# Optimization experiments

Hardware: AMD Instinct MI355X
Metric: run time of the kernel (lower is better)

Reference implementation:

```python
import jax, jax.numpy as jnp
import numpy as np

B, D, C = 512, 512, 100000
M1, M2, M3 = 1.0, 0.5, 0.0  # canonical ArcFace margins
EPS = 1e-12  # tf.nn.l2_normalize epsilon


def _l2norm(v, axis):
    return v * jax.lax.rsqrt(jnp.maximum(jnp.sum(v * v, axis=axis, keepdims=True), EPS))


def setup_inputs() -> dict:
    key = jax.random.key(0)
    k1, k2, k3 = jax.random.split(key, 3)
    x = jax.random.normal(k1, (B, D), dtype=jnp.float32)
    W = jax.random.normal(k2, (D, C), dtype=jnp.float32)
    label_idx = jax.random.randint(k3, (B,), 0, C, dtype=jnp.int32)
    return {"x": x, "W": W, "label_idx": label_idx}


def reference(x, W, label_idx):
    xn = _l2norm(x, axis=1)            # [B, D] unit embeddings
    Wn = _l2norm(W, axis=0)            # [D, C] unit class weights (norm=True fc)
    logits = xn @ Wn                   # [B, C] cosine similarities
    # gather target cosine per row (gather_nd over one-hot label)
    t = jnp.take_along_axis(logits, label_idx[:, None], axis=1)[:, 0]  # [B]
    # m1 == 1.0 -> skip angular scaling branch; m2 != 0 -> additive angular margin
    t = jnp.arccos(t) + M2
    # clamp to pi value-wise, straight-through gradient: t1 = t + pi - stop_grad(t)
    t = jnp.minimum(t, t + (jnp.pi - jax.lax.stop_gradient(t)))
    t = jnp.cos(t)
    onehot = jax.nn.one_hot(label_idx, C, dtype=logits.dtype)  # [B, C]
    out = logits * (1.0 - onehot) + t[:, None] * onehot
    out = out - onehot * M3
    return out
```

## Files before the change

### kernel.cpp

```cpp
#include <hip/hip_runtime.h>
#include <math.h>

#define BB 512
#define DD 512
#define CC 100000
#define MARGIN2 0.5f
#define PI_F 3.14159265358979323846f

#define BM 128
#define BN 128
#define BK 64
#define KSTEPS (DD / BK)
#define NPAN 782
#define GRID (4 * NPAN)

typedef __bf16 bf16x8 __attribute__((ext_vector_type(8)));
typedef float f32x4 __attribute__((ext_vector_type(4)));

static __device__ __forceinline__ unsigned short f2bf(float f) {
    union { float f; unsigned u; } v; v.f = f;
    unsigned r = v.u + 0x7FFFu + ((v.u >> 16) & 1u);
    return (unsigned short)(r >> 16);
}

static __device__ __forceinline__ int swz(int row, int kbyte) {
    return row * 128 + (kbyte ^ ((row & 7) << 4));
}

static __device__ __forceinline__ void gll16(const unsigned char* g, unsigned char* l) {
    __builtin_amdgcn_global_load_lds(
        (const __attribute__((address_space(1))) void*)g,
        (__attribute__((address_space(3))) void*)l, 16, 0, 0);
}

__global__ __launch_bounds__(256) void k_norm_x(const float* __restrict__ x,
                                                unsigned char* __restrict__ img) {
    const int lane = threadIdx.x & 63;
    const int row  = blockIdx.x * 4 + (threadIdx.x >> 6);
    const float* xr = x + (size_t)row * DD;
    float4 v0 = *(const float4*)(xr + lane * 4);
    float4 v1 = *(const float4*)(xr + lane * 4 + 256);
    float s = v0.x*v0.x + v0.y*v0.y + v0.z*v0.z + v0.w*v0.w
            + v1.x*v1.x + v1.y*v1.y + v1.z*v1.z + v1.w*v1.w;
    #pragma unroll
    for (int m = 32; m; m >>= 1) s += __shfl_xor(s, m, 64);
    float rs = rsqrtf(fmaxf(s, 1e-12f));
    ushort4 o0, o1;
    o0.x = f2bf(v0.x * rs); o0.y = f2bf(v0.y * rs);
    o0.z = f2bf(v0.z * rs); o0.w = f2bf(v0.w * rs);
    o1.x = f2bf(v1.x * rs); o1.y = f2bf(v1.y * rs);
    o1.z = f2bf(v1.z * rs); o1.w = f2bf(v1.w * rs);

    const int mb   = row >> 7;
    const int lrow = row & 127;
    const int k0   = lane * 4;
    const int t0   = k0 >> 6;
    const int c8   = (k0 >> 3) & 7;
    const int sub  = (k0 >> 2) & 1;
    const int base = (mb * 8 + t0) * 16384 + lrow * 128
                   + ((c8 * 16) ^ ((lrow & 7) << 4)) + sub * 8;
    *(ushort4*)(img + base)         = o0;
    *(ushort4*)(img + base + 65536) = o1;
}

#define ABUF 16384
#define LDSZ (2 * ABUF + 2 * 16384 + 512 + 512)

__global__ __launch_bounds__(512, 4) void k_gemm(const unsigned char* __restrict__ img,
                                                 const float* __restrict__ W,
                                                 const int* __restrict__ lab,
                                                 float* __restrict__ out) {
    __shared__ __align__(16) unsigned char LDS[LDSZ];
    unsigned char* bufA = LDS;
    unsigned char* bufB = LDS + 2 * ABUF;
    float* rn  = (float*)(LDS + 2 * ABUF + 32768);
    int*   labs = (int*)(LDS + 2 * ABUF + 32768 + 512);

    const int tid = threadIdx.x;
    const int bid = blockIdx.x;

    const int v  = (bid & 7) * 391 + (bid >> 3);
    const int mb = v & 3;
    const int nb = v >> 2;
    const int M0 = mb * BM;
    const int N0 = nb * BN;

    const int lane = tid & 63;
    const int wid  = tid >> 6;
    const int wm = wid >> 2;
    const int wn = wid & 3;
    const int lr = lane & 15;
    const int lg = lane >> 4;

    if (tid < 128) labs[tid] = lab[M0 + tid];

    int b_go[2], b_ld[2];
    #pragma unroll
    for (int i = 0; i < 2; ++i) {
        int s  = tid + i * 512;
        int n  = s & 127;
        int o  = s >> 7;
        int col = N0 + n;
        col = col < CC ? col : CC - 1;
        b_go[i] = o * 8 * CC + col;
        b_ld[i] = n * 128 + ((o * 16) ^ ((n & 7) << 4));
    }

    const unsigned char* imgA = img + mb * (8 * ABUF);
    const int lds_u = wid * 2048;

    float f0[2][8], f1[2][8], f2[2][8];
    float bsq[2] = {0.f, 0.f};

#define WAITV_(N) asm volatile("s_waitcnt vmcnt(" #N ")" ::: "memory")
#define WAITV(N) WAITV_(N)
#define SB() __builtin_amdgcn_sched_barrier(0)

#define LOAD_B(FR, T) do {                                                     \
    _Pragma("unroll")                                                          \
    for (int i = 0; i < 2; ++i) {                                              \
        const float* p = W + b_go[i] + (size_t)(T) * (BK * CC);                \
        _Pragma("unroll")                                                      \
        for (int j = 0; j < 8; ++j)                                            \
            FR[i][j] = p[(size_t)j * CC];                                      \
    } } while (0)

#define PACK_WRITE(FR, T) do {                                                 \
    unsigned char* dst = bufB + ((T) & 1) * 16384;                             \
    _Pragma("unroll")                                                          \
    for (int i = 0; i < 2; ++i) {                                              \
        _Pragma("unroll")                                                      \
        for (int j = 0; j < 8; ++j)                                            \
            bsq[i] += FR[i][j] * FR[i][j];                                     \
        uint4 w;                                                               \
        asm("v_cvt_pk_bf16_f32 %0, %1, %2" : "=v"(w.x) : "v"(FR[i][0]), "v"(FR[i][1])); \
        asm("v_cvt_pk_bf16_f32 %0, %1, %2" : "=v"(w.y) : "v"(FR[i][2]), "v"(FR[i][3])); \
        asm("v_cvt_pk_bf16_f32 %0, %1, %2" : "=v"(w.z) : "v"(FR[i][4]), "v"(FR[i][5])); \
        asm("v_cvt_pk_bf16_f32 %0, %1, %2" : "=v"(w.w) : "v"(FR[i][6]), "v"(FR[i][7])); \
        *(uint4*)(dst + b_ld[i]) = w;                                          \
    } } while (0)

#define GLL_A(T) do {                                                          \
    unsigned char* A_nxt = bufA + ((T) & 1) * ABUF;                            \
    const unsigned char* gsrc = imgA + (T) * ABUF;                             \
    gll16(gsrc + lds_u + lane * 16, A_nxt + lds_u);                            \
    gll16(gsrc + lds_u + 1024 + lane * 16, A_nxt + lds_u + 1024);              \
    } while (0)

#define COMPUTE(T) do {                                                        \
    const unsigned char* A_cur = bufA + ((T) & 1) * ABUF;                      \
    const unsigned char* B_cur = bufB + ((T) & 1) * 16384;                     \
    __builtin_amdgcn_s_setprio(1);                                             \
    _Pragma("unroll")                                                          \
    for (int ks = 0; ks < 2; ++ks) {                                           \
        bf16x8 af[4], bfr[2];                                                  \
        _Pragma("unroll")                                                      \
        for (int mf = 0; mf < 4; ++mf)                                         \
            af[mf] = *(const bf16x8*)(A_cur + swz(wm * 64 + mf * 16 + lr, ks * 64 + lg * 16)); \
        _Pragma("unroll")                                                      \
        for (int nf = 0; nf < 2; ++nf)                                         \
            bfr[nf] = *(const bf16x8*)(B_cur + swz(wn * 32 + nf * 16 + lr, ks * 64 + lg * 16)); \
        _Pragma("unroll")                                                      \
        for (int mf = 0; mf < 4; ++mf)                                         \
            _Pragma("unroll")                                                  \
            for (int nf = 0; nf < 2; ++nf)                                     \
                acc[mf][nf] = __builtin_amdgcn_mfma_f32_16x16x32_bf16(         \
                    bfr[nf], af[mf], acc[mf][nf], 0, 0, 0);                    \
    }                                                                          \
    __builtin_amdgcn_s_setprio(0);                                             \
    } while (0)

#define KBODY(T, FP, FN) do {                                                  \
    if ((T) + 1 < KSTEPS) GLL_A((T) + 1);         \
    if ((T) + 3 < KSTEPS) LOAD_B(FN, (T) + 3);                                 \
    COMPUTE(T);                                                                \
    if ((T) + 1 < KSTEPS) PACK_WRITE(FP, (T) + 1);                             \
    SB();                                                                      \
    if ((T) + 1 < KSTEPS) {                                                    \
        if ((T) + 3 < KSTEPS) { WAITV(16); } else { WAITV(0); }                \
        SB();                                                                  \
        asm volatile("s_waitcnt lgkmcnt(0)" ::: "memory"); SB();               \
        __builtin_amdgcn_s_barrier(); SB();                                    \
    } } while (0)

    f32x4 acc[4][2];
    #pragma unroll
    for (int mf = 0; mf < 4; ++mf)
        #pragma unroll
        for (int nf = 0; nf < 2; ++nf)
            acc[mf][nf] = (f32x4)0.f;

    LOAD_B(f0, 0);
    GLL_A(0);
    LOAD_B(f1, 1);
    PACK_WRITE(f0, 0);
    LOAD_B(f2, 2);
    SB();
    WAITV(32); SB();
    asm volatile("s_waitcnt lgkmcnt(0)" ::: "memory"); SB();
    __builtin_amdgcn_s_barrier(); SB();

    KBODY(0, f1, f0);
    KBODY(1, f2, f1);
    KBODY(2, f0, f2);
    KBODY(3, f1, f0);
    KBODY(4, f2, f1);
    KBODY(5, f0, f2);
    KBODY(6, f1, f0);
    KBODY(7, f2, f1);

    __syncthreads();
    float* part = (float*)bufB;
    #pragma unroll
    for (int i = 0; i < 2; ++i)
        part[tid + i * 512] = bsq[i];
    __syncthreads();
    if (tid < BN) {
        float s = 0.f;
        #pragma unroll
        for (int o = 0; o < 8; ++o)
            s += part[o * BN + tid];
        rn[tid] = rsqrtf(fmaxf(s, 1e-12f));
    }
    __syncthreads();

    float* stag = (float*)bufA;
    #pragma unroll
    for (int rd = 0; rd < 4; ++rd) {
        if (wm == (rd >> 1)) {
            #pragma unroll
            for (int f = 0; f < 2; ++f) {
                const int mf = (rd & 1) * 2 + f;
                const int ml = f * 16 + lr;
                #pragma unroll
                for (int nf = 0; nf < 2; ++nf) {
                    const int nl = wn * 32 + nf * 16 + lg * 4;
                    const f32x4 rn4 = *(const f32x4*)(rn + nl);
                    f32x4 o;
                    #pragma unroll
                    for (int r = 0; r < 4; ++r)
                        o[r] = acc[mf][nf][r] * rn4[r];
                    *(f32x4*)(stag + ml * 132 + nl) = o;
                }
            }
        }
        __syncthreads();
        if (tid < 32) {
            const int c   = labs[rd * 32 + tid];
            const int off = c - N0;
            if (off >= 0 && off < BN) {
                float val = stag[tid * 132 + off];
                val = fminf(fmaxf(val, -1.f), 1.f);
                float th = fminf(acosf(val) + MARGIN2, PI_F);
                stag[tid * 132 + off] = cosf(th);
            }
        }
        __syncthreads();
        #pragma unroll
        for (int j = tid; j < 1024; j += 512) {
            const int m = j >> 5;
            const int n = (j & 31) * 4;
            if (N0 + n + 4 <= CC) {
                f32x4 o = *(const f32x4*)(stag + m * 132 + n);
                __builtin_nontemporal_store(o,
                    (f32x4*)(out + (size_t)(M0 + rd * 32 + m) * CC + N0 + n));
            }
        }
        __syncthreads();
    }
}

extern "C" void kernel_launch(void* const* d_in, const int* in_sizes, int n_in,
                              void* d_out, int out_size, void* d_ws, size_t ws_size,
                              hipStream_t stream) {
    const float* x   = (const float*)d_in[0];
    const float* W   = (const float*)d_in[1];
    const int*   lab = (const int*)d_in[2];
    float* out = (float*)d_out;

    unsigned char* img = (unsigned char*)d_ws;

    k_norm_x<<<dim3(BB / 4), dim3(256), 0, stream>>>(x, img);
    k_gemm<<<dim3(GRID), dim3(512), 0, stream>>>(img, W, lab, out);
}
```

Before: 103.8 us.

## Load A fragments directly from global into registers, drop LDS A buffer

The normalized x matrix is now stored row-major in bf16, and each wave loads its MFMA A fragments straight from global memory into registers instead of staging them through swizzled LDS with global_load_lds. This frees LDS (the A double buffer is removed) and removes the LDS reads for A. The B prefetch depth drops from three register sets to two, and the explicit vmcnt waits are removed. The risk is exposed global latency on the A loads, now issued in the same k-step they are used, plus reduced W prefetch depth.

```diff
diff --git a/kernel.cpp b/kernel.cpp
--- a/kernel.cpp
+++ b/kernel.cpp
@@ -27,14 +27,8 @@
     return row * 128 + (kbyte ^ ((row & 7) << 4));
 }
 
-static __device__ __forceinline__ void gll16(const unsigned char* g, unsigned char* l) {
-    __builtin_amdgcn_global_load_lds(
-        (const __attribute__((address_space(1))) void*)g,
-        (__attribute__((address_space(3))) void*)l, 16, 0, 0);
-}
-
 __global__ __launch_bounds__(256) void k_norm_x(const float* __restrict__ x,
-                                                unsigned char* __restrict__ img) {
+                                                unsigned short* __restrict__ xnb) {
     const int lane = threadIdx.x & 63;
     const int row  = blockIdx.x * 4 + (threadIdx.x >> 6);
     const float* xr = x + (size_t)row * DD;
@@ -50,31 +44,20 @@
     o0.z = f2bf(v0.z * rs); o0.w = f2bf(v0.w * rs);
     o1.x = f2bf(v1.x * rs); o1.y = f2bf(v1.y * rs);
     o1.z = f2bf(v1.z * rs); o1.w = f2bf(v1.w * rs);
-
-    const int mb   = row >> 7;
-    const int lrow = row & 127;
-    const int k0   = lane * 4;
-    const int t0   = k0 >> 6;
-    const int c8   = (k0 >> 3) & 7;
-    const int sub  = (k0 >> 2) & 1;
-    const int base = (mb * 8 + t0) * 16384 + lrow * 128
-                   + ((c8 * 16) ^ ((lrow & 7) << 4)) + sub * 8;
-    *(ushort4*)(img + base)         = o0;
-    *(ushort4*)(img + base + 65536) = o1;
-}
-
-#define ABUF 16384
-#define LDSZ (2 * ABUF + 2 * 16384 + 512 + 512)
-
-__global__ __launch_bounds__(512, 4) void k_gemm(const unsigned char* __restrict__ img,
+    *(ushort4*)(xnb + (size_t)row * DD + lane * 4)       = o0;
+    *(ushort4*)(xnb + (size_t)row * DD + lane * 4 + 256) = o1;
+}
+
+#define LDSZ (2 * 16384 + 512 + 512)
+
+__global__ __launch_bounds__(512, 4) void k_gemm(const unsigned short* __restrict__ xnb,
                                                  const float* __restrict__ W,
                                                  const int* __restrict__ lab,
                                                  float* __restrict__ out) {
     __shared__ __align__(16) unsigned char LDS[LDSZ];
-    unsigned char* bufA = LDS;
-    unsigned char* bufB = LDS + 2 * ABUF;
-    float* rn  = (float*)(LDS + 2 * ABUF + 32768);
-    int*   labs = (int*)(LDS + 2 * ABUF + 32768 + 512);
+    unsigned char* bufB = LDS;
+    float* rn   = (float*)(LDS + 32768);
+    int*   labs = (int*)(LDS + 32768 + 512);
 
     const int tid = threadIdx.x;
     const int bid = blockIdx.x;
@@ -93,6 +76,11 @@
     const int lg = lane >> 4;
 
     if (tid < 128) labs[tid] = lab[M0 + tid];
+
+    const unsigned short* aptr0 = xnb + (size_t)(M0 + wm * 64 +  0 + lr) * DD + lg * 8;
+    const unsigned short* aptr1 = xnb + (size_t)(M0 + wm * 64 + 16 + lr) * DD + lg * 8;
+    const unsigned short* aptr2 = xnb + (size_t)(M0 + wm * 64 + 32 + lr) * DD + lg * 8;
+    const unsigned short* aptr3 = xnb + (size_t)(M0 + wm * 64 + 48 + lr) * DD + lg * 8;
 
     int b_go[2], b_ld[2];
     #pragma unroll
@@ -106,14 +94,10 @@
         b_ld[i] = n * 128 + ((o * 16) ^ ((n & 7) << 4));
     }
 
-    const unsigned char* imgA = img + mb * (8 * ABUF);
-    const int lds_u = wid * 2048;
-
-    float f0[2][8], f1[2][8], f2[2][8];
+    float f0[2][8], f1[2][8];
     float bsq[2] = {0.f, 0.f};
-
-#define WAITV_(N) asm volatile("s_waitcnt vmcnt(" #N ")" ::: "memory")
-#define WAITV(N) WAITV_(N)
+    bf16x8 af[4][2];
+
 #define SB() __builtin_amdgcn_sched_barrier(0)
 
 #define LOAD_B(FR, T) do {                                                     \
@@ -140,23 +124,23 @@
         *(uint4*)(dst + b_ld[i]) = w;                                          \
     } } while (0)
 
-#define GLL_A(T) do {                                                          \
-    unsigned char* A_nxt = bufA + ((T) & 1) * ABUF;                            \
-    const unsigned char* gsrc = imgA + (T) * ABUF;                             \
-    gll16(gsrc + lds_u + lane * 16, A_nxt + lds_u);                            \
-    gll16(gsrc + lds_u + 1024 + lane * 16, A_nxt + lds_u + 1024);              \
+#define LOAD_AF(T) do {                                                        \
+    af[0][0] = *(const bf16x8*)(aptr0 + (T) * 64);                             \
+    af[1][0] = *(const bf16x8*)(aptr1 + (T) * 64);                             \
+    af[2][0] = *(const bf16x8*)(aptr2 + (T) * 64);                             \
+    af[3][0] = *(const bf16x8*)(aptr3 + (T) * 64);                             \
+    af[0][1] = *(const bf16x8*)(aptr0 + (T) * 64 + 32);                        \
+    af[1][1] = *(const bf16x8*)(aptr1 + (T) * 64 + 32);                        \
+    af[2][1] = *(const bf16x8*)(aptr2 + (T) * 64 + 32);                        \
+    af[3][1] = *(const bf16x8*)(aptr3 + (T) * 64 + 32);                        \
     } while (0)
 
 #define COMPUTE(T) do {                                                        \
-    const unsigned char* A_cur = bufA + ((T) & 1) * ABUF;                      \
     const unsigned char* B_cur = bufB + ((T) & 1) * 16384;                     \
     __builtin_amdgcn_s_setprio(1);                                             \
     _Pragma("unroll")                                                          \
     for (int ks = 0; ks < 2; ++ks) {                                           \
-        bf16x8 af[4], bfr[2];                                                  \
-        _Pragma("unroll")                                                      \
-        for (int mf = 0; mf < 4; ++mf)                                         \
-            af[mf] = *(const bf16x8*)(A_cur + swz(wm * 64 + mf * 16 + lr, ks * 64 + lg * 16)); \
+        bf16x8 bfr[2];                                                         \
         _Pragma("unroll")                                                      \
         for (int nf = 0; nf < 2; ++nf)                                         \
             bfr[nf] = *(const bf16x8*)(B_cur + swz(wn * 32 + nf * 16 + lr, ks * 64 + lg * 16)); \
@@ -165,20 +149,18 @@
             _Pragma("unroll")                                                  \
             for (int nf = 0; nf < 2; ++nf)                                     \
                 acc[mf][nf] = __builtin_amdgcn_mfma_f32_16x16x32_bf16(         \
-                    bfr[nf], af[mf], acc[mf][nf], 0, 0, 0);                    \
+                    bfr[nf], af[mf][ks], acc[mf][nf], 0, 0, 0);                \
     }                                                                          \
     __builtin_amdgcn_s_setprio(0);                                             \
     } while (0)
 
 #define KBODY(T, FP, FN) do {                                                  \
-    if ((T) + 1 < KSTEPS) GLL_A((T) + 1);         \
-    if ((T) + 3 < KSTEPS) LOAD_B(FN, (T) + 3);                                 \
+    LOAD_AF(T);                                                                \
+    if ((T) + 2 < KSTEPS) LOAD_B(FN, (T) + 2);                                 \
     COMPUTE(T);                                                                \
     if ((T) + 1 < KSTEPS) PACK_WRITE(FP, (T) + 1);                             \
     SB();                                                                      \
     if ((T) + 1 < KSTEPS) {                                                    \
-        if ((T) + 3 < KSTEPS) { WAITV(16); } else { WAITV(0); }                \
-        SB();                                                                  \
         asm volatile("s_waitcnt lgkmcnt(0)" ::: "memory"); SB();               \
         __builtin_amdgcn_s_barrier(); SB();                                    \
     } } while (0)
@@ -191,23 +173,20 @@
             acc[mf][nf] = (f32x4)0.f;
 
     LOAD_B(f0, 0);
-    GLL_A(0);
+    PACK_WRITE(f0, 0);
     LOAD_B(f1, 1);
-    PACK_WRITE(f0, 0);
-    LOAD_B(f2, 2);
     SB();
-    WAITV(32); SB();
     asm volatile("s_waitcnt lgkmcnt(0)" ::: "memory"); SB();
     __builtin_amdgcn_s_barrier(); SB();
 
     KBODY(0, f1, f0);
-    KBODY(1, f2, f1);
-    KBODY(2, f0, f2);
-    KBODY(3, f1, f0);
-    KBODY(4, f2, f1);
-    KBODY(5, f0, f2);
+    KBODY(1, f0, f1);
+    KBODY(2, f1, f0);
+    KBODY(3, f0, f1);
+    KBODY(4, f1, f0);
+    KBODY(5, f0, f1);
     KBODY(6, f1, f0);
-    KBODY(7, f2, f1);
+    KBODY(7, f0, f1);
 
     __syncthreads();
     float* part = (float*)bufB;
@@ -224,7 +203,7 @@
     }
     __syncthreads();
 
-    float* stag = (float*)bufA;
+    float* stag = (float*)LDS;
     #pragma unroll
     for (int rd = 0; rd < 4; ++rd) {
         if (wm == (rd >> 1)) {
@@ -278,8 +257,8 @@
     const int*   lab = (const int*)d_in[2];
     float* out = (float*)d_out;
 
-    unsigned char* img = (unsigned char*)d_ws;
-
-    k_norm_x<<<dim3(BB / 4), dim3(256), 0, stream>>>(x, img);
-    k_gemm<<<dim3(GRID), dim3(512), 0, stream>>>(img, W, lab, out);
-}
+    unsigned short* xnb = (unsigned short*)d_ws;
+
+    k_norm_x<<<dim3(BB / 4), dim3(256), 0, stream>>>(x, xnb);
+    k_gemm<<<dim3(GRID), dim3(512), 0, stream>>>(xnb, W, lab, out);
+}
```

After: 230.8 us. 2.22x slower.
